# Optimization experiments

Measured on AMD Instinct MI355X. Metric: run time of the kernel, lower is better.

Reference implementation:

```python
import jax, jax.numpy as jnp
import numpy as np

N = 100000   # nodes
E = 1200000  # edges
D = 64       # emb_dim
XIN = 18     # x_dim + node_dim
XD = 16      # x_dim (output)
ED = 1       # edge_dim
L = 4        # num message-passing layers
G = 8        # graphs in batch (for global_mean_pool)


def setup_inputs() -> dict:
    key = jax.random.key(0)
    ks = iter(jax.random.split(key, 64))
    def nrm(shape, s=0.05):
        return jax.random.normal(next(ks), shape, dtype=jnp.float32) * s
    inp = {}
    inp["x"] = jax.random.normal(next(ks), (N, XIN), dtype=jnp.float32)
    inp["edge_attr"] = jax.random.normal(next(ks), (E, ED), dtype=jnp.float32)
    inp["W_in"] = nrm((XIN, D)); inp["b_in"] = jnp.zeros((D,), jnp.float32)
    # per-layer stacked params (leading dim L)
    inp["msg_W1"] = nrm((L, 2 * D + ED, D)); inp["msg_b1"] = jnp.zeros((L, D), jnp.float32)
    inp["msg_g1"] = jnp.ones((L, D), jnp.float32); inp["msg_be1"] = jnp.zeros((L, D), jnp.float32)
    inp["msg_W2"] = nrm((L, D, D)); inp["msg_b2"] = jnp.zeros((L, D), jnp.float32)
    inp["msg_g2"] = jnp.ones((L, D), jnp.float32); inp["msg_be2"] = jnp.zeros((L, D), jnp.float32)
    inp["upd_W1"] = nrm((L, 2 * D, D)); inp["upd_b1"] = jnp.zeros((L, D), jnp.float32)
    inp["upd_g1"] = jnp.ones((L, D), jnp.float32); inp["upd_be1"] = jnp.zeros((L, D), jnp.float32)
    inp["upd_W2"] = nrm((L, D, D)); inp["upd_b2"] = jnp.zeros((L, D), jnp.float32)
    inp["upd_g2"] = jnp.ones((L, D), jnp.float32); inp["upd_be2"] = jnp.zeros((L, D), jnp.float32)
    inp["reward_W"] = nrm((D, D)); inp["reward_b"] = jnp.zeros((D,), jnp.float32)
    inp["rout_W"] = nrm((D, 1)); inp["rout_b"] = jnp.zeros((1,), jnp.float32)
    inp["pred_W"] = nrm((D, D)); inp["pred_b"] = jnp.zeros((D,), jnp.float32)
    inp["pout_W"] = nrm((D, XD)); inp["pout_b"] = jnp.zeros((XD,), jnp.float32)
    inp["edge_index"] = jax.random.randint(next(ks), (2, E), 0, N)
    inp["batch"] = jnp.sort(jax.random.randint(next(ks), (N,), 0, G))
    return inp


def _bn(x, g, b, eps=1e-5):
    # BatchNorm1d in training mode: batch mean + biased variance
    m = jnp.mean(x, axis=0)
    v = jnp.mean((x - m) ** 2, axis=0)
    return (x - m) * jax.lax.rsqrt(v + eps) * g + b


def _mlp(x, W1, b1, g1, be1, W2, b2, g2, be2):
    h = jax.nn.relu(_bn(x @ W1 + b1, g1, be1))
    return jax.nn.relu(_bn(h @ W2 + b2, g2, be2))


def _forward(x, edge_attr, W_in, b_in,
             msg_W1, msg_b1, msg_g1, msg_be1, msg_W2, msg_b2, msg_g2, msg_be2,
             upd_W1, upd_b1, upd_g1, upd_be1, upd_W2, upd_b2, upd_g2, upd_be2,
             reward_W, reward_b, rout_W, rout_b, pred_W, pred_b, pout_W, pout_b,
             edge_index, batch):
    src = edge_index[0]  # j (source)
    dst = edge_index[1]  # i (target); PyG default flow source_to_target
    n = x.shape[0]
    h = x @ W_in + b_in
    for l in range(L):
        # message: gather + concat + MLP(psi)
        m = jnp.concatenate([h[dst], h[src], edge_attr], axis=-1)  # (E, 2D+ED)
        m = _mlp(m, msg_W1[l], msg_b1[l], msg_g1[l], msg_be1[l],
                 msg_W2[l], msg_b2[l], msg_g2[l], msg_be2[l])
        # aggregate: scatter-add to target nodes
        agg = jax.ops.segment_sum(m, dst, num_segments=n)  # (N, D)
        # update: concat + MLP(phi); residual add from outer network
        u = jnp.concatenate([h, agg], axis=-1)
        h = h + _mlp(u, upd_W1[l], upd_b1[l], upd_g1[l], upd_be1[l],
                     upd_W2[l], upd_b2[l], upd_g2[l], upd_be2[l])
    # reward head (computed in the original forward but not returned)
    h_reward = h @ reward_W + reward_b
    cnt = jax.ops.segment_sum(jnp.ones((n,), h.dtype), batch, num_segments=G)
    h_graph = jax.ops.segment_sum(h_reward, batch, num_segments=G) / jnp.maximum(cnt, 1.0)[:, None]
    _out_reward = h_graph @ rout_W + rout_b  # unused, matches original return
    # prediction head
    x_out = jax.nn.relu(h @ pred_W + pred_b) @ pout_W + pout_b  # (N, XD)
    return x_out


def reference(x, edge_attr, W_in, b_in,
              msg_W1, msg_b1, msg_g1, msg_be1, msg_W2, msg_b2, msg_g2, msg_be2,
              upd_W1, upd_b1, upd_g1, upd_be1, upd_W2, upd_b2, upd_g2, upd_be2,
              reward_W, reward_b, rout_W, rout_b, pred_W, pred_b, pout_W, pout_b,
              edge_index, batch):
    return _forward(x, edge_attr, W_in, b_in,
                    msg_W1, msg_b1, msg_g1, msg_be1, msg_W2, msg_b2, msg_g2, msg_be2,
                    upd_W1, upd_b1, upd_g1, upd_be1, upd_W2, upd_b2, upd_g2, upd_be2,
                    reward_W, reward_b, rout_W, rout_b, pred_W, pred_b, pout_W, pout_b,
                    edge_index, batch)
```

## Files before the change

kernel.cpp:

```cpp
#include <hip/hip_runtime.h>
#include <hip/hip_fp16.h>

typedef unsigned short u16;
typedef unsigned int u32;
typedef __attribute__((ext_vector_type(8))) unsigned short us8;
typedef __attribute__((ext_vector_type(8))) _Float16 f16x8;
typedef __attribute__((ext_vector_type(4))) float f32x4;

#define EPS 1e-5f

__device__ __forceinline__ float h2f(u16 h){ __half v; *(u16*)&v = h; return __half2float(v); }
__device__ __forceinline__ u16 f2h(float f){ __half v = __float2half(f); return *(u16*)&v; }

__global__ __launch_bounds__(256) void k_in(const float* __restrict__ x,
    const float* __restrict__ Win, const float* __restrict__ bin,
    float* __restrict__ h, int N){
  __shared__ float Ws[18][64];
  __shared__ float xs[64][20];
  int tid = threadIdx.x;
  for (int i = tid; i < 18*64; i += 256) Ws[i>>6][i&63] = Win[i];
  int row0 = blockIdx.x * 64;
  for (int i = tid; i < 64*18; i += 256){
    int r = i/18, k = i - r*18;
    int row = row0 + r;
    xs[r][k] = (row < N) ? x[(size_t)row*18 + k] : 0.f;
  }
  __syncthreads();
  int rq = tid >> 4, dq = tid & 15;
  float4 b4 = *(const float4*)(bin + dq*4);
  float acc[4][4];
  #pragma unroll
  for (int j=0;j<4;j++){ acc[j][0]=b4.x; acc[j][1]=b4.y; acc[j][2]=b4.z; acc[j][3]=b4.w; }
  for (int k=0;k<18;k++){
    float4 wv = *(const float4*)&Ws[k][dq*4];
    #pragma unroll
    for (int j=0;j<4;j++){
      float v = xs[rq*4+j][k];
      acc[j][0]+=v*wv.x; acc[j][1]+=v*wv.y; acc[j][2]+=v*wv.z; acc[j][3]+=v*wv.w;
    }
  }
  #pragma unroll
  for (int j=0;j<4;j++){
    int row = row0 + rq*4 + j;
    if (row < N)
      *(float4*)(h + (size_t)row*64 + dq*4) = make_float4(acc[j][0],acc[j][1],acc[j][2],acc[j][3]);
  }
}

__global__ __launch_bounds__(256) void k_pq(const float* __restrict__ h,
    const float* __restrict__ A, const float* __restrict__ B,
    u16* __restrict__ P, u16* __restrict__ Q, int N){
  __shared__ float hs[64][68];
  __shared__ float As[64][64];
  __shared__ float Bs[64][64];
  int tid = threadIdx.x;
  for (int i = tid; i < 4096; i += 256){ As[i>>6][i&63] = A[i]; Bs[i>>6][i&63] = B[i]; }
  int row0 = blockIdx.x*64;
  for (int i = tid; i < 4096; i += 256){
    int r = i>>6, k = i&63; int row = row0+r;
    hs[r][k] = (row<N)? h[(size_t)row*64+k] : 0.f;
  }
  __syncthreads();
  int rq = tid>>4, dq = tid&15;
  float ap[4][4]={}, aq[4][4]={};
  for (int k=0;k<64;k+=4){
    float4 hv[4];
    #pragma unroll
    for (int j=0;j<4;j++) hv[j] = *(const float4*)&hs[rq*4+j][k];
    #pragma unroll
    for (int kk=0;kk<4;kk++){
      float4 av = *(const float4*)&As[k+kk][dq*4];
      float4 bv = *(const float4*)&Bs[k+kk][dq*4];
      #pragma unroll
      for (int j=0;j<4;j++){
        float v = ((const float*)&hv[j])[kk];
        ap[j][0]+=v*av.x; ap[j][1]+=v*av.y; ap[j][2]+=v*av.z; ap[j][3]+=v*av.w;
        aq[j][0]+=v*bv.x; aq[j][1]+=v*bv.y; aq[j][2]+=v*bv.z; aq[j][3]+=v*bv.w;
      }
    }
  }
  #pragma unroll
  for (int j=0;j<4;j++){
    int row = row0 + rq*4 + j;
    if (row<N){
      ushort4 pk, qk;
      pk.x=f2h(ap[j][0]); pk.y=f2h(ap[j][1]); pk.z=f2h(ap[j][2]); pk.w=f2h(ap[j][3]);
      qk.x=f2h(aq[j][0]); qk.y=f2h(aq[j][1]); qk.z=f2h(aq[j][2]); qk.w=f2h(aq[j][3]);
      *(ushort4*)(P+(size_t)row*64+dq*4) = pk;
      *(ushort4*)(Q+(size_t)row*64+dq*4) = qk;
    }
  }
}

__global__ __launch_bounds__(256) void k_hist(const int* __restrict__ ei, int* __restrict__ cnt, int E){
  int e = blockIdx.x*256 + threadIdx.x;
  if (e < E) atomicAdd(&cnt[ei[E+e]], 1);
}

__global__ __launch_bounds__(256) void k_scan_a(const int* __restrict__ cnt, int* __restrict__ rp,
    int* __restrict__ bsum, int N){
  __shared__ int sm[256];
  int tid = threadIdx.x;
  int i0 = blockIdx.x*1024 + tid*4;
  int v0 = (i0+0<N)? cnt[i0+0]:0;
  int v1 = (i0+1<N)? cnt[i0+1]:0;
  int v2 = (i0+2<N)? cnt[i0+2]:0;
  int v3 = (i0+3<N)? cnt[i0+3]:0;
  int s = v0+v1+v2+v3;
  sm[tid] = s; __syncthreads();
  for (int ofs=1; ofs<256; ofs<<=1){
    int v = sm[tid];
    if (tid >= ofs) v += sm[tid-ofs];
    __syncthreads(); sm[tid] = v; __syncthreads();
  }
  int base = sm[tid] - s;
  int a0 = base+v0, a1 = a0+v1, a2 = a1+v2, a3 = a2+v3;
  if (i0+0<N) rp[i0+0]=a0;
  if (i0+1<N) rp[i0+1]=a1;
  if (i0+2<N) rp[i0+2]=a2;
  if (i0+3<N) rp[i0+3]=a3;
  if (tid==255) bsum[blockIdx.x] = sm[255];
}

__global__ void k_scan_b(int* __restrict__ bsum, int NB){
  if (threadIdx.x==0){
    int run = 0;
    for (int b=0;b<NB;b++){ int t = bsum[b]; bsum[b] = run; run += t; }
  }
}

__global__ __launch_bounds__(256) void k_scan_c(const int* __restrict__ cnt, int* __restrict__ rp,
    int* __restrict__ wr, const int* __restrict__ bsum, int N, int E){
  int tid = threadIdx.x;
  int i0 = blockIdx.x*1024 + tid*4;
  int off = bsum[blockIdx.x];
  #pragma unroll
  for (int j=0;j<4;j++){
    int i = i0+j;
    if (i<N){ int ex = off + rp[i] - cnt[i]; rp[i] = ex; wr[i] = ex; }
  }
  if (blockIdx.x==0 && tid==0) rp[N] = E;
}

__global__ __launch_bounds__(256) void k_perm(const int* __restrict__ ei, const float* __restrict__ ea,
    int* __restrict__ wr, int2* __restrict__ seS, int E){
  int e = blockIdx.x*256 + threadIdx.x;
  if (e < E){
    int dn = ei[E+e];
    int pos = atomicAdd(&wr[dn], 1);
    seS[pos] = make_int2(ei[e], __float_as_int(ea[e]));
  }
}

__global__ __launch_bounds__(256) void k_t1s(const u16* __restrict__ P, const u16* __restrict__ Q,
    const int2* __restrict__ seS, const int* __restrict__ rp,
    const float* __restrict__ c1, const float* __restrict__ b1,
    u16* __restrict__ t, float* __restrict__ stats, int N){
  int tid = threadIdx.x;
  int lane = tid & 63, w = tid >> 6;
  int sub = lane >> 5;
  int dl = (lane & 31) * 2;
  float cv0 = c1[dl], cv1 = c1[dl+1];
  float bv0 = b1[dl], bv1 = b1[dl+1];
  float s0 = 0.f, s1 = 0.f, qs0 = 0.f, qs1 = 0.f;
  for (int n = blockIdx.x*4 + w; n < N; n += gridDim.x*4){
    int a = rp[n], b = rp[n+1];
    u32 pp = *(const u32*)(P + (size_t)n*64 + dl);
    float p0 = h2f((u16)(pp & 0xffffu)) + bv0;
    float p1 = h2f((u16)(pp >> 16)) + bv1;
    int p = a + sub;
    for (; p + 2 < b; p += 4){
      int2 seA = seS[p];
      int2 seB = seS[p+2];
      u32 qA = *(const u32*)(Q + (size_t)seA.x*64 + dl);
      u32 qB = *(const u32*)(Q + (size_t)seB.x*64 + dl);
      float eaA = __int_as_float(seA.y), eaB = __int_as_float(seB.y);
      float tA0 = p0 + h2f((u16)(qA & 0xffffu)) + eaA*cv0;
      float tA1 = p1 + h2f((u16)(qA >> 16)) + eaA*cv1;
      float tB0 = p0 + h2f((u16)(qB & 0xffffu)) + eaB*cv0;
      float tB1 = p1 + h2f((u16)(qB >> 16)) + eaB*cv1;
      *(u32*)(t + (size_t)p*64 + dl) = (u32)f2h(tA0) | ((u32)f2h(tA1) << 16);
      *(u32*)(t + (size_t)(p+2)*64 + dl) = (u32)f2h(tB0) | ((u32)f2h(tB1) << 16);
      s0 += tA0 + tB0; s1 += tA1 + tB1;
      qs0 += tA0*tA0 + tB0*tB0; qs1 += tA1*tA1 + tB1*tB1;
    }
    for (; p < b; p += 2){
      int2 se = seS[p];
      u32 qq = *(const u32*)(Q + (size_t)se.x*64 + dl);
      float ea = __int_as_float(se.y);
      float t0 = p0 + h2f((u16)(qq & 0xffffu)) + ea*cv0;
      float t1 = p1 + h2f((u16)(qq >> 16)) + ea*cv1;
      *(u32*)(t + (size_t)p*64 + dl) = (u32)f2h(t0) | ((u32)f2h(t1) << 16);
      s0 += t0; s1 += t1; qs0 += t0*t0; qs1 += t1*t1;
    }
  }
  __shared__ float sS[8][64], qS[8][64];
  int idx = w*2 + sub;
  sS[idx][dl] = s0; sS[idx][dl+1] = s1;
  qS[idx][dl] = qs0; qS[idx][dl+1] = qs1;
  __syncthreads();
  if (tid < 64){
    float ts = 0.f, tq = 0.f;
    #pragma unroll
    for (int r=0;r<8;r++){ ts += sS[r][tid]; tq += qS[r][tid]; }
    atomicAdd(&stats[tid], ts);
    atomicAdd(&stats[64+tid], tq);
  }
}

__global__ __launch_bounds__(256) void k_m2s(u16* __restrict__ t,
    const float* __restrict__ g1, const float* __restrict__ be1, const float* __restrict__ stats1,
    const float* __restrict__ W2, const float* __restrict__ b2,
    float* __restrict__ stats2, int E, float invE){
  __shared__ _Float16 yL[128][72];
  __shared__ _Float16 wL[64][72];
  __shared__ float scS[64], shS[64], b2S[64];
  int tid = threadIdx.x;
  if (tid < 64){
    float m = stats1[tid]*invE;
    float v = stats1[64+tid]*invE - m*m;
    float sc = g1[tid]*rsqrtf(v + EPS);
    scS[tid] = sc; shS[tid] = be1[tid] - m*sc;
    b2S[tid] = b2[tid];
  }
  for (int i = tid; i < 4096; i += 256){
    int k = i >> 6, n = i & 63;
    wL[n][k] = (_Float16)W2[i];
  }
  __syncthreads();
  int lane = tid & 63, wv = tid >> 6;
  int arow = lane & 15;
  int kgrp = lane >> 4;
  int srow = tid >> 1, sc0 = (tid & 1)*32;
  float ssum[4] = {}, ssq[4] = {};
  int ntiles = (E + 127) >> 7;
  for (int tile = blockIdx.x; tile < ntiles; tile += gridDim.x){
    int e0 = tile << 7;
    {
      int p = e0 + srow;
      if (p < E){
        const u16* src = t + (size_t)p*64 + sc0;
        #pragma unroll
        for (int c=0;c<4;c++){
          f16x8 a = *(const f16x8*)(src + c*8);
          f16x8 v;
          #pragma unroll
          for (int j=0;j<8;j++){
            int dd = sc0 + c*8 + j;
            v[j] = (_Float16)fmaxf((float)a[j]*scS[dd] + shS[dd], 0.f);
          }
          *(f16x8*)&yL[srow][sc0 + c*8] = v;
        }
      } else {
        f16x8 z;
        #pragma unroll
        for (int j=0;j<8;j++) z[j] = (_Float16)0.f;
        #pragma unroll
        for (int c=0;c<4;c++) *(f16x8*)&yL[srow][sc0 + c*8] = z;
      }
    }
    __syncthreads();
    f32x4 acc[2][4];
    #pragma unroll
    for (int mf=0; mf<2; mf++){
      int row = 32*wv + 16*mf + arow;
      f16x8 a0 = *(const f16x8*)&yL[row][8*kgrp];
      f16x8 a1 = *(const f16x8*)&yL[row][32 + 8*kgrp];
      #pragma unroll
      for (int c=0;c<4;c++){
        f16x8 b0 = *(const f16x8*)&wL[16*c + arow][8*kgrp];
        f16x8 b1 = *(const f16x8*)&wL[16*c + arow][32 + 8*kgrp];
        f32x4 d = {0.f,0.f,0.f,0.f};
        d = __builtin_amdgcn_mfma_f32_16x16x32_f16(a0, b0, d, 0, 0, 0);
        d = __builtin_amdgcn_mfma_f32_16x16x32_f16(a1, b1, d, 0, 0, 0);
        acc[mf][c] = d;
      }
    }
    __syncthreads();
    #pragma unroll
    for (int mf=0; mf<2; mf++){
      #pragma unroll
      for (int c=0;c<4;c++){
        int col = 16*c + arow;
        float bb = b2S[col];
        #pragma unroll
        for (int r=0;r<4;r++){
          int e = e0 + 32*wv + 16*mf + 4*kgrp + r;
          if (e < E){
            float v = acc[mf][c][r] + bb;
            t[(size_t)e*64 + col] = f2h(v);
            ssum[c] += v; ssq[c] += v*v;
          }
        }
      }
    }
  }
  __syncthreads();
  float* red = (float*)yL;
  #pragma unroll
  for (int c=0;c<4;c++) red[c*256 + tid] = ssum[c];
  __syncthreads();
  if (tid < 64){
    int cc = tid >> 4;
    float s = 0.f;
    for (int g=0; g<16; g++) s += red[cc*256 + g*16 + (tid & 15)];
    atomicAdd(&stats2[tid], s);
  }
  __syncthreads();
  #pragma unroll
  for (int c=0;c<4;c++) red[c*256 + tid] = ssq[c];
  __syncthreads();
  if (tid < 64){
    int cc = tid >> 4;
    float s = 0.f;
    for (int g=0; g<16; g++) s += red[cc*256 + g*16 + (tid & 15)];
    atomicAdd(&stats2[64+tid], s);
  }
}

__global__ __launch_bounds__(256) void k_agg(const u16* __restrict__ t2, const int* __restrict__ rp,
    const float* __restrict__ g2, const float* __restrict__ be2, const float* __restrict__ stats2,
    float* __restrict__ agg, int N, float invE){
  __shared__ float scS[64], shS[64];
  int tid = threadIdx.x;
  if (tid < 64){
    float m = stats2[tid]*invE;
    float v = stats2[64+tid]*invE - m*m;
    float sc = g2[tid]*rsqrtf(v+EPS);
    scS[tid] = sc; shS[tid] = be2[tid] - m*sc;
  }
  __syncthreads();
  int lane = tid & 63, w = tid >> 6;
  int sub = lane >> 5;
  int dl = (lane & 31) * 2;
  float sc0 = scS[dl], sc1 = scS[dl+1], sh0 = shS[dl], sh1 = shS[dl+1];
  for (int n = blockIdx.x*4 + w; n < N; n += gridDim.x*4){
    int a = rp[n], b = rp[n+1];
    float a0 = 0.f, a1 = 0.f;
    int p = a + sub;
    for (; p + 2 < b; p += 4){
      u32 vA = *(const u32*)(t2 + (size_t)p*64 + dl);
      u32 vB = *(const u32*)(t2 + (size_t)(p+2)*64 + dl);
      a0 += fmaxf(h2f((u16)(vA & 0xffffu))*sc0 + sh0, 0.f)
          + fmaxf(h2f((u16)(vB & 0xffffu))*sc0 + sh0, 0.f);
      a1 += fmaxf(h2f((u16)(vA >> 16))*sc1 + sh1, 0.f)
          + fmaxf(h2f((u16)(vB >> 16))*sc1 + sh1, 0.f);
    }
    for (; p < b; p += 2){
      u32 vA = *(const u32*)(t2 + (size_t)p*64 + dl);
      a0 += fmaxf(h2f((u16)(vA & 0xffffu))*sc0 + sh0, 0.f);
      a1 += fmaxf(h2f((u16)(vA >> 16))*sc1 + sh1, 0.f);
    }
    a0 += __shfl_xor(a0, 32);
    a1 += __shfl_xor(a1, 32);
    if (sub == 0)
      *(float2*)(agg + (size_t)n*64 + dl) = make_float2(a0, a1);
  }
}

__global__ __launch_bounds__(256) void k_s1(const u16* __restrict__ P, const u16* __restrict__ Q,
    const float* __restrict__ ea, const int* __restrict__ ei,
    const float* __restrict__ c1, const float* __restrict__ b1,
    float* __restrict__ stats, int E){
  int tid = threadIdx.x;
  int d = tid & 63, w = tid >> 6;
  float cv = c1[d], bv = b1[d];
  float s = 0.f, sq = 0.f;
  for (int e = blockIdx.x*4 + w; e < E; e += gridDim.x*4){
    int dn = ei[E+e], sn = ei[e];
    float t = h2f(P[(size_t)dn*64+d]) + h2f(Q[(size_t)sn*64+d]) + ea[e]*cv + bv;
    s += t; sq += t*t;
  }
  __shared__ float sS[4][64], qS[4][64];
  sS[w][d] = s; qS[w][d] = sq;
  __syncthreads();
  if (tid < 64){
    float ts = sS[0][tid]+sS[1][tid]+sS[2][tid]+sS[3][tid];
    float tq = qS[0][tid]+qS[1][tid]+qS[2][tid]+qS[3][tid];
    atomicAdd(&stats[tid], ts);
    atomicAdd(&stats[64+tid], tq);
  }
}

__global__ __launch_bounds__(256) void k_m2b(const u16* __restrict__ P, const u16* __restrict__ Q,
    const float* __restrict__ ea, const int* __restrict__ ei,
    const float* __restrict__ c1, const float* __restrict__ b1,
    const float* __restrict__ g1, const float* __restrict__ be1,
    const float* __restrict__ stats1,
    const float* __restrict__ W2, const float* __restrict__ b2,
    float* __restrict__ stats2, int E, float invE){
  __shared__ float ys[64][68];
  __shared__ float Ws[64][64];
  __shared__ float scS[64], c1S[64], bS[64], b2S[64];
  int tid = threadIdx.x;
  if (tid < 64){
    float m = stats1[tid]*invE;
    float v = stats1[64+tid]*invE - m*m;
    float sc = g1[tid]*rsqrtf(v + EPS);
    float sh = be1[tid] - m*sc;
    scS[tid] = sc;
    c1S[tid] = c1[tid]*sc;
    bS[tid]  = b1[tid]*sc + sh;
    b2S[tid] = b2[tid];
  }
  for (int i=tid;i<4096;i+=256) Ws[i>>6][i&63] = W2[i];
  __syncthreads();
  int rq = tid>>4, dq = tid&15;
  float ssum[4]={}, ssq[4]={};
  int ntiles = (E+63)>>6;
  for (int tile = blockIdx.x; tile < ntiles; tile += gridDim.x){
    int e0 = tile<<6;
    for (int i = tid; i < 4096; i += 256){
      int el = i>>6, dd = i&63;
      int e = e0 + el;
      float y = 0.f;
      if (e < E){
        int dn = ei[E+e], sn = ei[e];
        float t = (h2f(P[(size_t)dn*64+dd]) + h2f(Q[(size_t)sn*64+dd]))*scS[dd] + ea[e]*c1S[dd] + bS[dd];
        y = fmaxf(t, 0.f);
      }
      ys[el][dd] = y;
    }
    __syncthreads();
    float acc[4][4];
    float4 b4 = *(const float4*)&b2S[dq*4];
    #pragma unroll
    for (int j=0;j<4;j++){ acc[j][0]=b4.x; acc[j][1]=b4.y; acc[j][2]=b4.z; acc[j][3]=b4.w; }
    for (int k=0;k<64;k+=4){
      float4 hv[4];
      #pragma unroll
      for (int j=0;j<4;j++) hv[j] = *(const float4*)&ys[rq*4+j][k];
      #pragma unroll
      for (int kk=0;kk<4;kk++){
        float4 wv = *(const float4*)&Ws[k+kk][dq*4];
        #pragma unroll
        for (int j=0;j<4;j++){
          float v = ((const float*)&hv[j])[kk];
          acc[j][0]+=v*wv.x; acc[j][1]+=v*wv.y; acc[j][2]+=v*wv.z; acc[j][3]+=v*wv.w;
        }
      }
    }
    #pragma unroll
    for (int j=0;j<4;j++){
      int e = e0 + rq*4 + j;
      if (e < E){
        #pragma unroll
        for (int c=0;c<4;c++){ float v=acc[j][c]; ssum[c]+=v; ssq[c]+=v*v; }
      }
    }
    __syncthreads();
  }
  float* red = &ys[0][0];
  #pragma unroll
  for (int c=0;c<4;c++) red[rq*64 + dq*4 + c] = ssum[c];
  __syncthreads();
  if (tid < 64){
    float t=0.f;
    for (int r=0;r<16;r++) t += red[r*64+tid];
    atomicAdd(&stats2[tid], t);
  }
  __syncthreads();
  #pragma unroll
  for (int c=0;c<4;c++) red[rq*64 + dq*4 + c] = ssq[c];
  __syncthreads();
  if (tid < 64){
    float t=0.f;
    for (int r=0;r<16;r++) t += red[r*64+tid];
    atomicAdd(&stats2[64+tid], t);
  }
}

__global__ __launch_bounds__(256) void k_sc_rec(const u16* __restrict__ P, const u16* __restrict__ Q,
    const float* __restrict__ ea, const int* __restrict__ ei,
    const float* __restrict__ c1, const float* __restrict__ b1,
    const float* __restrict__ g1, const float* __restrict__ be1, const float* __restrict__ stats1,
    const float* __restrict__ W2, const float* __restrict__ b2,
    const float* __restrict__ g2, const float* __restrict__ be2, const float* __restrict__ stats2,
    float* __restrict__ agg, int E, float invE){
  __shared__ float ys[64][68];
  __shared__ float Ws[64][64];
  __shared__ float scS[64], c1S[64], bS[64];
  __shared__ float s2S[64], h2S[64], b2S[64];
  int tid = threadIdx.x;
  if (tid < 64){
    float m = stats1[tid]*invE;
    float v = stats1[64+tid]*invE - m*m;
    float sc = g1[tid]*rsqrtf(v + EPS);
    scS[tid] = sc;
    c1S[tid] = c1[tid]*sc;
    bS[tid]  = b1[tid]*sc + be1[tid] - m*sc;
    float m2 = stats2[tid]*invE;
    float v2 = stats2[64+tid]*invE - m2*m2;
    float sc2 = g2[tid]*rsqrtf(v2+EPS);
    s2S[tid] = sc2; h2S[tid] = be2[tid] - m2*sc2;
    b2S[tid] = b2[tid];
  }
  for (int i=tid;i<4096;i+=256) Ws[i>>6][i&63] = W2[i];
  __syncthreads();
  int rq = tid>>4, dq = tid&15;
  int ntiles = (E+63)>>6;
  for (int tile = blockIdx.x; tile < ntiles; tile += gridDim.x){
    int e0 = tile<<6;
    for (int i = tid; i < 4096; i += 256){
      int el = i>>6, dd = i&63;
      int e = e0 + el;
      float y = 0.f;
      if (e < E){
        int dn = ei[E+e], sn = ei[e];
        float t = (h2f(P[(size_t)dn*64+dd]) + h2f(Q[(size_t)sn*64+dd]))*scS[dd] + ea[e]*c1S[dd] + bS[dd];
        y = fmaxf(t, 0.f);
      }
      ys[el][dd] = y;
    }
    __syncthreads();
    float acc[4][4];
    float4 b4 = *(const float4*)&b2S[dq*4];
    #pragma unroll
    for (int j=0;j<4;j++){ acc[j][0]=b4.x; acc[j][1]=b4.y; acc[j][2]=b4.z; acc[j][3]=b4.w; }
    for (int k=0;k<64;k+=4){
      float4 hv[4];
      #pragma unroll
      for (int j=0;j<4;j++) hv[j] = *(const float4*)&ys[rq*4+j][k];
      #pragma unroll
      for (int kk=0;kk<4;kk++){
        float4 wv = *(const float4*)&Ws[k+kk][dq*4];
        #pragma unroll
        for (int j=0;j<4;j++){
          float v = ((const float*)&hv[j])[kk];
          acc[j][0]+=v*wv.x; acc[j][1]+=v*wv.y; acc[j][2]+=v*wv.z; acc[j][3]+=v*wv.w;
        }
      }
    }
    float4 sc4 = *(const float4*)&s2S[dq*4];
    float4 sh4 = *(const float4*)&h2S[dq*4];
    #pragma unroll
    for (int j=0;j<4;j++){
      int e = e0 + rq*4 + j;
      if (e < E){
        int dn = ei[E+e];
        float y0 = fmaxf(acc[j][0]*sc4.x + sh4.x, 0.f);
        float y1 = fmaxf(acc[j][1]*sc4.y + sh4.y, 0.f);
        float y2 = fmaxf(acc[j][2]*sc4.z + sh4.z, 0.f);
        float y3 = fmaxf(acc[j][3]*sc4.w + sh4.w, 0.f);
        atomicAdd(&agg[(size_t)dn*64 + dq*4    ], y0);
        atomicAdd(&agg[(size_t)dn*64 + dq*4 + 1], y1);
        atomicAdd(&agg[(size_t)dn*64 + dq*4 + 2], y2);
        atomicAdd(&agg[(size_t)dn*64 + dq*4 + 3], y3);
      }
    }
    __syncthreads();
  }
}

__global__ __launch_bounds__(256) void k_up1(const float* __restrict__ h, const float* __restrict__ agg,
    const float* __restrict__ U1, const float* __restrict__ b1u,
    float* __restrict__ tn, float* __restrict__ stats3, int N){
  __shared__ float ins[64][68];
  __shared__ float Ws[64][64];
  int tid = threadIdx.x;
  int rq = tid>>4, dq = tid&15;
  int row0 = blockIdx.x*64;
  float4 b4 = *(const float4*)(b1u + dq*4);
  float acc[4][4];
  #pragma unroll
  for (int j=0;j<4;j++){ acc[j][0]=b4.x; acc[j][1]=b4.y; acc[j][2]=b4.z; acc[j][3]=b4.w; }
  for (int p=0;p<2;p++){
    const float* src = p ? agg : h;
    for (int i=tid;i<4096;i+=256){
      int r=i>>6,k=i&63; int row=row0+r;
      ins[r][k] = (row<N)? src[(size_t)row*64+k] : 0.f;
    }
    for (int i=tid;i<4096;i+=256) Ws[i>>6][i&63] = U1[p*4096 + i];
    __syncthreads();
    for (int k=0;k<64;k+=4){
      float4 hv[4];
      #pragma unroll
      for (int j=0;j<4;j++) hv[j] = *(const float4*)&ins[rq*4+j][k];
      #pragma unroll
      for (int kk=0;kk<4;kk++){
        float4 wv = *(const float4*)&Ws[k+kk][dq*4];
        #pragma unroll
        for (int j=0;j<4;j++){
          float v = ((const float*)&hv[j])[kk];
          acc[j][0]+=v*wv.x; acc[j][1]+=v*wv.y; acc[j][2]+=v*wv.z; acc[j][3]+=v*wv.w;
        }
      }
    }
    __syncthreads();
  }
  float ssum[4]={}, ssq[4]={};
  #pragma unroll
  for (int j=0;j<4;j++){
    int row = row0 + rq*4 + j;
    if (row<N){
      *(float4*)(tn+(size_t)row*64+dq*4) = make_float4(acc[j][0],acc[j][1],acc[j][2],acc[j][3]);
      #pragma unroll
      for (int c=0;c<4;c++){ float v=acc[j][c]; ssum[c]+=v; ssq[c]+=v*v; }
    }
  }
  float* red = &ins[0][0];
  #pragma unroll
  for (int c=0;c<4;c++) red[rq*64 + dq*4 + c] = ssum[c];
  __syncthreads();
  if (tid < 64){
    float t=0.f; for (int r=0;r<16;r++) t += red[r*64+tid];
    atomicAdd(&stats3[tid], t);
  }
  __syncthreads();
  #pragma unroll
  for (int c=0;c<4;c++) red[rq*64 + dq*4 + c] = ssq[c];
  __syncthreads();
  if (tid < 64){
    float t=0.f; for (int r=0;r<16;r++) t += red[r*64+tid];
    atomicAdd(&stats3[64+tid], t);
  }
}

__global__ __launch_bounds__(256) void k_up2(float* __restrict__ tn,
    const float* __restrict__ g3, const float* __restrict__ be3, const float* __restrict__ stats3,
    const float* __restrict__ U2, const float* __restrict__ b2u,
    float* __restrict__ stats4, int N, float invN){
  __shared__ float ys[64][68];
  __shared__ float Ws[64][64];
  __shared__ float scS[64], shS[64], bS[64];
  int tid = threadIdx.x;
  if (tid < 64){
    float m = stats3[tid]*invN;
    float v = stats3[64+tid]*invN - m*m;
    float sc = g3[tid]*rsqrtf(v+EPS);
    scS[tid] = sc; shS[tid] = be3[tid] - m*sc; bS[tid] = b2u[tid];
  }
  for (int i=tid;i<4096;i+=256) Ws[i>>6][i&63] = U2[i];
  int row0 = blockIdx.x*64;
  __syncthreads();
  for (int i=tid;i<4096;i+=256){
    int r=i>>6,k=i&63; int row=row0+r;
    float y = 0.f;
    if (row<N) y = fmaxf(tn[(size_t)row*64+k]*scS[k] + shS[k], 0.f);
    ys[r][k] = y;
  }
  __syncthreads();
  int rq = tid>>4, dq = tid&15;
  float4 b4 = *(const float4*)&bS[dq*4];
  float acc[4][4];
  #pragma unroll
  for (int j=0;j<4;j++){ acc[j][0]=b4.x; acc[j][1]=b4.y; acc[j][2]=b4.z; acc[j][3]=b4.w; }
  for (int k=0;k<64;k+=4){
    float4 hv[4];
    #pragma unroll
    for (int j=0;j<4;j++) hv[j] = *(const float4*)&ys[rq*4+j][k];
    #pragma unroll
    for (int kk=0;kk<4;kk++){
      float4 wv = *(const float4*)&Ws[k+kk][dq*4];
      #pragma unroll
      for (int j=0;j<4;j++){
        float v = ((const float*)&hv[j])[kk];
        acc[j][0]+=v*wv.x; acc[j][1]+=v*wv.y; acc[j][2]+=v*wv.z; acc[j][3]+=v*wv.w;
      }
    }
  }
  float ssum[4]={}, ssq[4]={};
  #pragma unroll
  for (int j=0;j<4;j++){
    int row = row0 + rq*4 + j;
    if (row<N){
      *(float4*)(tn+(size_t)row*64+dq*4) = make_float4(acc[j][0],acc[j][1],acc[j][2],acc[j][3]);
      #pragma unroll
      for (int c=0;c<4;c++){ float v=acc[j][c]; ssum[c]+=v; ssq[c]+=v*v; }
    }
  }
  __syncthreads();
  float* red = &ys[0][0];
  #pragma unroll
  for (int c=0;c<4;c++) red[rq*64 + dq*4 + c] = ssum[c];
  __syncthreads();
  if (tid < 64){
    float t=0.f; for (int r=0;r<16;r++) t += red[r*64+tid];
    atomicAdd(&stats4[tid], t);
  }
  __syncthreads();
  #pragma unroll
  for (int c=0;c<4;c++) red[rq*64 + dq*4 + c] = ssq[c];
  __syncthreads();
  if (tid < 64){
    float t=0.f; for (int r=0;r<16;r++) t += red[r*64+tid];
    atomicAdd(&stats4[64+tid], t);
  }
}

__global__ __launch_bounds__(256) void k_res_pq(float* __restrict__ h, const float* __restrict__ tn,
    const float* __restrict__ g4, const float* __restrict__ be4, const float* __restrict__ stats4,
    const float* __restrict__ A, const float* __restrict__ B,
    u16* __restrict__ P, u16* __restrict__ Q, int N, float invN){
  __shared__ float hs[64][68];
  __shared__ float As[64][64];
  __shared__ float Bs[64][64];
  __shared__ float scS[64], shS[64];
  int tid = threadIdx.x;
  if (tid < 64){
    float m = stats4[tid]*invN;
    float v = stats4[64+tid]*invN - m*m;
    float sc = g4[tid]*rsqrtf(v+EPS);
    scS[tid] = sc; shS[tid] = be4[tid] - m*sc;
  }
  for (int i = tid; i < 4096; i += 256){ As[i>>6][i&63] = A[i]; Bs[i>>6][i&63] = B[i]; }
  int row0 = blockIdx.x*64;
  __syncthreads();
  for (int i = tid; i < 4096; i += 256){
    int r = i>>6, k = i&63; int row = row0+r;
    float hv = 0.f;
    if (row<N){
      hv = h[(size_t)row*64+k] + fmaxf(tn[(size_t)row*64+k]*scS[k] + shS[k], 0.f);
      h[(size_t)row*64+k] = hv;
    }
    hs[r][k] = hv;
  }
  __syncthreads();
  int rq = tid>>4, dq = tid&15;
  float ap[4][4]={}, aq[4][4]={};
  for (int k=0;k<64;k+=4){
    float4 hv[4];
    #pragma unroll
    for (int j=0;j<4;j++) hv[j] = *(const float4*)&hs[rq*4+j][k];
    #pragma unroll
    for (int kk=0;kk<4;kk++){
      float4 av = *(const float4*)&As[k+kk][dq*4];
      float4 bv = *(const float4*)&Bs[k+kk][dq*4];
      #pragma unroll
      for (int j=0;j<4;j++){
        float v = ((const float*)&hv[j])[kk];
        ap[j][0]+=v*av.x; ap[j][1]+=v*av.y; ap[j][2]+=v*av.z; ap[j][3]+=v*av.w;
        aq[j][0]+=v*bv.x; aq[j][1]+=v*bv.y; aq[j][2]+=v*bv.z; aq[j][3]+=v*bv.w;
      }
    }
  }
  #pragma unroll
  for (int j=0;j<4;j++){
    int row = row0 + rq*4 + j;
    if (row<N){
      ushort4 pk, qk;
      pk.x=f2h(ap[j][0]); pk.y=f2h(ap[j][1]); pk.z=f2h(ap[j][2]); pk.w=f2h(ap[j][3]);
      qk.x=f2h(aq[j][0]); qk.y=f2h(aq[j][1]); qk.z=f2h(aq[j][2]); qk.w=f2h(aq[j][3]);
      *(ushort4*)(P+(size_t)row*64+dq*4) = pk;
      *(ushort4*)(Q+(size_t)row*64+dq*4) = qk;
    }
  }
}

__global__ __launch_bounds__(256) void k_res_head(const float* __restrict__ h, const float* __restrict__ tn,
    const float* __restrict__ g4, const float* __restrict__ be4, const float* __restrict__ stats4,
    const float* __restrict__ Wp, const float* __restrict__ bp,
    const float* __restrict__ Wo, const float* __restrict__ bo,
    float* __restrict__ out, int N, float invN){
  __shared__ float hs[64][68];
  __shared__ float Wps[64][64];
  __shared__ float ps[64][68];
  __shared__ float Wos[64][16];
  __shared__ float scS[64], shS[64];
  int tid = threadIdx.x;
  if (tid < 64){
    float m = stats4[tid]*invN;
    float v = stats4[64+tid]*invN - m*m;
    float sc = g4[tid]*rsqrtf(v+EPS);
    scS[tid] = sc; shS[tid] = be4[tid] - m*sc;
  }
  for (int i=tid;i<4096;i+=256) Wps[i>>6][i&63] = Wp[i];
  for (int i=tid;i<1024;i+=256) Wos[i>>4][i&15] = Wo[i];
  int row0 = blockIdx.x*64;
  __syncthreads();
  for (int i = tid; i < 4096; i += 256){
    int r = i>>6, k = i&63; int row = row0+r;
    float hv = 0.f;
    if (row<N)
      hv = h[(size_t)row*64+k] + fmaxf(tn[(size_t)row*64+k]*scS[k] + shS[k], 0.f);
    hs[r][k] = hv;
  }
  __syncthreads();
  int rq = tid>>4, dq = tid&15;
  float4 b4 = *(const float4*)(bp + dq*4);
  float acc[4][4];
  #pragma unroll
  for (int j=0;j<4;j++){ acc[j][0]=b4.x; acc[j][1]=b4.y; acc[j][2]=b4.z; acc[j][3]=b4.w; }
  for (int k=0;k<64;k+=4){
    float4 hv[4];
    #pragma unroll
    for (int j=0;j<4;j++) hv[j] = *(const float4*)&hs[rq*4+j][k];
    #pragma unroll
    for (int kk=0;kk<4;kk++){
      float4 wv = *(const float4*)&Wps[k+kk][dq*4];
      #pragma unroll
      for (int j=0;j<4;j++){
        float v = ((const float*)&hv[j])[kk];
        acc[j][0]+=v*wv.x; acc[j][1]+=v*wv.y; acc[j][2]+=v*wv.z; acc[j][3]+=v*wv.w;
      }
    }
  }
  #pragma unroll
  for (int j=0;j<4;j++){
    *(float4*)&ps[rq*4+j][dq*4] = make_float4(fmaxf(acc[j][0],0.f), fmaxf(acc[j][1],0.f),
                                              fmaxf(acc[j][2],0.f), fmaxf(acc[j][3],0.f));
  }
  __syncthreads();
  int f = tid & 15;
  float bof = bo[f];
  float acc2[4] = {bof, bof, bof, bof};
  for (int k=0;k<64;k++){
    float wv = Wos[k][f];
    #pragma unroll
    for (int j=0;j<4;j++) acc2[j] += ps[rq*4+j][k]*wv;
  }
  #pragma unroll
  for (int j=0;j<4;j++){
    int row = row0 + rq*4 + j;
    if (row<N) out[(size_t)row*16 + f] = acc2[j];
  }
}

extern "C" void kernel_launch(void* const* d_in, const int* in_sizes, int n_in,
                              void* d_out, int out_size, void* d_ws, size_t ws_size,
                              hipStream_t stream){
  const float* x    = (const float*)d_in[0];
  const float* eatt = (const float*)d_in[1];
  const float* Win  = (const float*)d_in[2];
  const float* bin  = (const float*)d_in[3];
  const float* mW1  = (const float*)d_in[4];
  const float* mb1  = (const float*)d_in[5];
  const float* mg1  = (const float*)d_in[6];
  const float* mbe1 = (const float*)d_in[7];
  const float* mW2  = (const float*)d_in[8];
  const float* mb2  = (const float*)d_in[9];
  const float* mg2  = (const float*)d_in[10];
  const float* mbe2 = (const float*)d_in[11];
  const float* uW1  = (const float*)d_in[12];
  const float* ub1  = (const float*)d_in[13];
  const float* ug1  = (const float*)d_in[14];
  const float* ube1 = (const float*)d_in[15];
  const float* uW2  = (const float*)d_in[16];
  const float* ub2  = (const float*)d_in[17];
  const float* ug2  = (const float*)d_in[18];
  const float* ube2 = (const float*)d_in[19];
  const float* predW = (const float*)d_in[24];
  const float* predb = (const float*)d_in[25];
  const float* poutW = (const float*)d_in[26];
  const float* poutb = (const float*)d_in[27];
  const int*   ei    = (const int*)d_in[28];

  const int N = in_sizes[0] / 18;
  const int E = in_sizes[1];

  size_t nodeB = (size_t)N * 64 * sizeof(float);
  size_t halfB = (size_t)N * 64 * sizeof(u16);
  size_t t2B   = (size_t)E * 64 * sizeof(u16);
  size_t statsB = 16 * 128 * sizeof(float);
  int NB = (N + 1023)/1024;
  size_t csrB = (size_t)E*8 + (size_t)(N+1)*4 + (size_t)N*4 + (size_t)N*4 + 4096*4;

  bool planA = ws_size >= nodeB + 2*halfB + nodeB + t2B + csrB + statsB;

  char* w = (char*)d_ws;
  float* h = (float*)w; w += nodeB;
  u16* P = (u16*)w; w += halfB;
  u16* Q = (u16*)w; w += halfB;
  float* agg = (float*)w; w += nodeB;
  float* tn = agg;
  u16*  t2 = nullptr;
  int2* seS = nullptr;
  int *rp=nullptr, *cnt=nullptr, *wrp=nullptr, *bsum=nullptr;
  float* stats;
  if (planA){
    t2   = (u16*)w;  w += t2B;
    seS  = (int2*)w; w += (size_t)E*8;
    rp   = (int*)w;  w += (size_t)(N+1)*4;
    cnt  = (int*)w;  w += (size_t)N*4;
    wrp  = (int*)w;  w += (size_t)N*4;
    bsum = (int*)w;  w += 4096*4;
    stats = (float*)w;
  } else {
    stats = (float*)w;
  }

  hipMemsetAsync(stats, 0, statsB, stream);

  int nb = (N + 63)/64;
  float invE = 1.0f/(float)E, invN = 1.0f/(float)N;

  k_in<<<nb, 256, 0, stream>>>(x, Win, bin, h, N);
  k_pq<<<nb, 256, 0, stream>>>(h, mW1, mW1 + 4096, P, Q, N);

  if (planA){
    hipMemsetAsync(cnt, 0, (size_t)N*4, stream);
    k_hist<<<(E+255)/256, 256, 0, stream>>>(ei, cnt, E);
    k_scan_a<<<NB, 256, 0, stream>>>(cnt, rp, bsum, N);
    k_scan_b<<<1, 64, 0, stream>>>(bsum, NB);
    k_scan_c<<<NB, 256, 0, stream>>>(cnt, rp, wrp, bsum, N, E);
    k_perm<<<(E+255)/256, 256, 0, stream>>>(ei, eatt, wrp, seS, E);
  }

  for (int l = 0; l < 4; ++l){
    float* s1 = stats + (l*4+0)*128;
    float* s2 = stats + (l*4+1)*128;
    float* s3 = stats + (l*4+2)*128;
    float* s4 = stats + (l*4+3)*128;
    const float* A  = mW1 + (size_t)l*8256;
    const float* c1 = A + 8192;
    if (planA){
      k_t1s<<<2048, 256, 0, stream>>>(P, Q, seS, rp, c1, mb1 + l*64, t2, s1, N);
      k_m2s<<<2048, 256, 0, stream>>>(t2, mg1 + l*64, mbe1 + l*64, s1,
                                      mW2 + (size_t)l*4096, mb2 + l*64, s2, E, invE);
      k_agg<<<2048, 256, 0, stream>>>(t2, rp, mg2 + l*64, mbe2 + l*64, s2, agg, N, invE);
    } else {
      k_s1<<<2048, 256, 0, stream>>>(P, Q, eatt, ei, c1, mb1 + l*64, s1, E);
      k_m2b<<<1024, 256, 0, stream>>>(P, Q, eatt, ei, c1, mb1 + l*64, mg1 + l*64, mbe1 + l*64,
                                      s1, mW2 + (size_t)l*4096, mb2 + l*64, s2, E, invE);
      hipMemsetAsync(agg, 0, nodeB, stream);
      k_sc_rec<<<1024, 256, 0, stream>>>(P, Q, eatt, ei, c1, mb1 + l*64, mg1 + l*64, mbe1 + l*64,
                                         s1, mW2 + (size_t)l*4096, mb2 + l*64,
                                         mg2 + l*64, mbe2 + l*64, s2, agg, E, invE);
    }
    k_up1<<<nb, 256, 0, stream>>>(h, agg, uW1 + (size_t)l*8192, ub1 + l*64, tn, s3, N);
    k_up2<<<nb, 256, 0, stream>>>(tn, ug1 + l*64, ube1 + l*64, s3, uW2 + (size_t)l*4096,
                                  ub2 + l*64, s4, N, invN);
    if (l < 3){
      const float* An = mW1 + (size_t)(l+1)*8256;
      k_res_pq<<<nb, 256, 0, stream>>>(h, tn, ug2 + l*64, ube2 + l*64, s4,
                                       An, An + 4096, P, Q, N, invN);
    } else {
      k_res_head<<<nb, 256, 0, stream>>>(h, tn, ug2 + l*64, ube2 + l*64, s4,
                                         predW, predb, poutW, poutb, (float*)d_out, N, invN);
    }
  }
}
```

Before: 2.166 ms.

## Port node update and P/Q projection kernels to fp16 MFMA

Rewrites k_up1, k_up2 and k_res_pq to stage inputs and transposed weights in LDS as fp16 and compute the 64x64 GEMMs with 16x16x32 MFMA instructions instead of scalar fp32 FMAs. Loads are vectorized per row, and the BN stats reduction is remapped to the MFMA output layout. This cuts ALU time in the node-side kernels. In exchange it adds fp16 rounding of h/agg inputs and weights, and it leaves the dominant edge-message kernel unchanged.

```diff
diff --git a/kernel.cpp b/kernel.cpp
--- a/kernel.cpp
+++ b/kernel.cpp
@@ -11,6 +11,7 @@
 
 __device__ __forceinline__ float h2f(u16 h){ __half v; *(u16*)&v = h; return __half2float(v); }
 __device__ __forceinline__ u16 f2h(float f){ __half v = __float2half(f); return *(u16*)&v; }
+__device__ __forceinline__ u32 pkh(float a, float b){ return (u32)f2h(a) | ((u32)f2h(b) << 16); }
 
 __global__ __launch_bounds__(256) void k_in(const float* __restrict__ x,
     const float* __restrict__ Win, const float* __restrict__ bin,
@@ -555,64 +556,87 @@
 __global__ __launch_bounds__(256) void k_up1(const float* __restrict__ h, const float* __restrict__ agg,
     const float* __restrict__ U1, const float* __restrict__ b1u,
     float* __restrict__ tn, float* __restrict__ stats3, int N){
-  __shared__ float ins[64][68];
-  __shared__ float Ws[64][64];
-  int tid = threadIdx.x;
-  int rq = tid>>4, dq = tid&15;
-  int row0 = blockIdx.x*64;
-  float4 b4 = *(const float4*)(b1u + dq*4);
-  float acc[4][4];
-  #pragma unroll
-  for (int j=0;j<4;j++){ acc[j][0]=b4.x; acc[j][1]=b4.y; acc[j][2]=b4.z; acc[j][3]=b4.w; }
-  for (int p=0;p<2;p++){
-    const float* src = p ? agg : h;
-    for (int i=tid;i<4096;i+=256){
-      int r=i>>6,k=i&63; int row=row0+r;
-      ins[r][k] = (row<N)? src[(size_t)row*64+k] : 0.f;
-    }
-    for (int i=tid;i<4096;i+=256) Ws[i>>6][i&63] = U1[p*4096 + i];
-    __syncthreads();
-    for (int k=0;k<64;k+=4){
-      float4 hv[4];
-      #pragma unroll
-      for (int j=0;j<4;j++) hv[j] = *(const float4*)&ins[rq*4+j][k];
-      #pragma unroll
-      for (int kk=0;kk<4;kk++){
-        float4 wv = *(const float4*)&Ws[k+kk][dq*4];
-        #pragma unroll
-        for (int j=0;j<4;j++){
-          float v = ((const float*)&hv[j])[kk];
-          acc[j][0]+=v*wv.x; acc[j][1]+=v*wv.y; acc[j][2]+=v*wv.z; acc[j][3]+=v*wv.w;
-        }
-      }
-    }
-    __syncthreads();
-  }
+  __shared__ _Float16 yL[64][136];
+  __shared__ _Float16 wL[64][136];
+  __shared__ float bS[64];
+  int tid = threadIdx.x;
+  if (tid < 64) bS[tid] = b1u[tid];
+  for (int i = tid; i < 8192; i += 256){
+    int k = i >> 6, n = i & 63;
+    wL[n][k] = (_Float16)U1[i];
+  }
+  int row0 = blockIdx.x * 64;
+  int srow = tid >> 2, sc0 = (tid & 3) * 16;
+  {
+    int row = row0 + srow;
+    if (row < N){
+      #pragma unroll
+      for (int c=0;c<4;c++){
+        float4 v = *(const float4*)(h + (size_t)row*64 + sc0 + 4*c);
+        *(u32*)&yL[srow][sc0+4*c]   = pkh(v.x, v.y);
+        *(u32*)&yL[srow][sc0+4*c+2] = pkh(v.z, v.w);
+      }
+      #pragma unroll
+      for (int c=0;c<4;c++){
+        float4 v = *(const float4*)(agg + (size_t)row*64 + sc0 + 4*c);
+        *(u32*)&yL[srow][64+sc0+4*c]   = pkh(v.x, v.y);
+        *(u32*)&yL[srow][64+sc0+4*c+2] = pkh(v.z, v.w);
+      }
+    } else {
+      #pragma unroll
+      for (int c=0;c<4;c++){
+        *(u32*)&yL[srow][sc0+4*c] = 0u; *(u32*)&yL[srow][sc0+4*c+2] = 0u;
+        *(u32*)&yL[srow][64+sc0+4*c] = 0u; *(u32*)&yL[srow][64+sc0+4*c+2] = 0u;
+      }
+    }
+  }
+  __syncthreads();
+  int lane = tid & 63, wv = tid >> 6;
+  int arow = lane & 15, kgrp = lane >> 4;
+  f16x8 a[4];
+  #pragma unroll
+  for (int kk=0;kk<4;kk++) a[kk] = *(const f16x8*)&yL[16*wv + arow][32*kk + 8*kgrp];
   float ssum[4]={}, ssq[4]={};
   #pragma unroll
-  for (int j=0;j<4;j++){
-    int row = row0 + rq*4 + j;
-    if (row<N){
-      *(float4*)(tn+(size_t)row*64+dq*4) = make_float4(acc[j][0],acc[j][1],acc[j][2],acc[j][3]);
-      #pragma unroll
-      for (int c=0;c<4;c++){ float v=acc[j][c]; ssum[c]+=v; ssq[c]+=v*v; }
-    }
-  }
-  float* red = &ins[0][0];
-  #pragma unroll
-  for (int c=0;c<4;c++) red[rq*64 + dq*4 + c] = ssum[c];
-  __syncthreads();
-  if (tid < 64){
-    float t=0.f; for (int r=0;r<16;r++) t += red[r*64+tid];
-    atomicAdd(&stats3[tid], t);
-  }
-  __syncthreads();
-  #pragma unroll
-  for (int c=0;c<4;c++) red[rq*64 + dq*4 + c] = ssq[c];
-  __syncthreads();
-  if (tid < 64){
-    float t=0.f; for (int r=0;r<16;r++) t += red[r*64+tid];
-    atomicAdd(&stats3[64+tid], t);
+  for (int c=0;c<4;c++){
+    f32x4 d = {0.f,0.f,0.f,0.f};
+    #pragma unroll
+    for (int kk=0;kk<4;kk++){
+      f16x8 b = *(const f16x8*)&wL[16*c + arow][32*kk + 8*kgrp];
+      d = __builtin_amdgcn_mfma_f32_16x16x32_f16(a[kk], b, d, 0, 0, 0);
+    }
+    int col = 16*c + arow;
+    float bb = bS[col];
+    #pragma unroll
+    for (int r=0;r<4;r++){
+      int row = row0 + 16*wv + 4*kgrp + r;
+      if (row < N){
+        float v = d[r] + bb;
+        tn[(size_t)row*64 + col] = v;
+        ssum[c]+=v; ssq[c]+=v*v;
+      }
+    }
+  }
+  __syncthreads();
+  float* red = (float*)yL;
+  #pragma unroll
+  for (int c=0;c<4;c++) red[c*256 + tid] = ssum[c];
+  __syncthreads();
+  if (tid < 64){
+    int cc = tid >> 4;
+    float s = 0.f;
+    for (int g=0; g<16; g++) s += red[cc*256 + g*16 + (tid & 15)];
+    atomicAdd(&stats3[tid], s);
+  }
+  __syncthreads();
+  #pragma unroll
+  for (int c=0;c<4;c++) red[c*256 + tid] = ssq[c];
+  __syncthreads();
+  if (tid < 64){
+    int cc = tid >> 4;
+    float s = 0.f;
+    for (int g=0; g<16; g++) s += red[cc*256 + g*16 + (tid & 15)];
+    atomicAdd(&stats3[64+tid], s);
   }
 }
 
@@ -620,8 +644,8 @@
     const float* __restrict__ g3, const float* __restrict__ be3, const float* __restrict__ stats3,
     const float* __restrict__ U2, const float* __restrict__ b2u,
     float* __restrict__ stats4, int N, float invN){
-  __shared__ float ys[64][68];
-  __shared__ float Ws[64][64];
+  __shared__ _Float16 yL[64][72];
+  __shared__ _Float16 wL[64][72];
   __shared__ float scS[64], shS[64], bS[64];
   int tid = threadIdx.x;
   if (tid < 64){
@@ -630,61 +654,79 @@
     float sc = g3[tid]*rsqrtf(v+EPS);
     scS[tid] = sc; shS[tid] = be3[tid] - m*sc; bS[tid] = b2u[tid];
   }
-  for (int i=tid;i<4096;i+=256) Ws[i>>6][i&63] = U2[i];
-  int row0 = blockIdx.x*64;
-  __syncthreads();
-  for (int i=tid;i<4096;i+=256){
-    int r=i>>6,k=i&63; int row=row0+r;
-    float y = 0.f;
-    if (row<N) y = fmaxf(tn[(size_t)row*64+k]*scS[k] + shS[k], 0.f);
-    ys[r][k] = y;
-  }
-  __syncthreads();
-  int rq = tid>>4, dq = tid&15;
-  float4 b4 = *(const float4*)&bS[dq*4];
-  float acc[4][4];
-  #pragma unroll
-  for (int j=0;j<4;j++){ acc[j][0]=b4.x; acc[j][1]=b4.y; acc[j][2]=b4.z; acc[j][3]=b4.w; }
-  for (int k=0;k<64;k+=4){
-    float4 hv[4];
-    #pragma unroll
-    for (int j=0;j<4;j++) hv[j] = *(const float4*)&ys[rq*4+j][k];
-    #pragma unroll
-    for (int kk=0;kk<4;kk++){
-      float4 wv = *(const float4*)&Ws[k+kk][dq*4];
-      #pragma unroll
-      for (int j=0;j<4;j++){
-        float v = ((const float*)&hv[j])[kk];
-        acc[j][0]+=v*wv.x; acc[j][1]+=v*wv.y; acc[j][2]+=v*wv.z; acc[j][3]+=v*wv.w;
-      }
-    }
-  }
+  for (int i = tid; i < 4096; i += 256){
+    int k = i >> 6, n = i & 63;
+    wL[n][k] = (_Float16)U2[i];
+  }
+  __syncthreads();
+  int row0 = blockIdx.x * 64;
+  int srow = tid >> 2, sc0 = (tid & 3) * 16;
+  {
+    int row = row0 + srow;
+    if (row < N){
+      #pragma unroll
+      for (int c=0;c<4;c++){
+        float4 v = *(const float4*)(tn + (size_t)row*64 + sc0 + 4*c);
+        int d0 = sc0 + 4*c;
+        float y0 = fmaxf(v.x*scS[d0  ] + shS[d0  ], 0.f);
+        float y1 = fmaxf(v.y*scS[d0+1] + shS[d0+1], 0.f);
+        float y2 = fmaxf(v.z*scS[d0+2] + shS[d0+2], 0.f);
+        float y3 = fmaxf(v.w*scS[d0+3] + shS[d0+3], 0.f);
+        *(u32*)&yL[srow][d0]   = pkh(y0, y1);
+        *(u32*)&yL[srow][d0+2] = pkh(y2, y3);
+      }
+    } else {
+      #pragma unroll
+      for (int c=0;c<4;c++){
+        *(u32*)&yL[srow][sc0+4*c] = 0u; *(u32*)&yL[srow][sc0+4*c+2] = 0u;
+      }
+    }
+  }
+  __syncthreads();
+  int lane = tid & 63, wv = tid >> 6;
+  int arow = lane & 15, kgrp = lane >> 4;
+  f16x8 a0 = *(const f16x8*)&yL[16*wv + arow][8*kgrp];
+  f16x8 a1 = *(const f16x8*)&yL[16*wv + arow][32 + 8*kgrp];
   float ssum[4]={}, ssq[4]={};
   #pragma unroll
-  for (int j=0;j<4;j++){
-    int row = row0 + rq*4 + j;
-    if (row<N){
-      *(float4*)(tn+(size_t)row*64+dq*4) = make_float4(acc[j][0],acc[j][1],acc[j][2],acc[j][3]);
-      #pragma unroll
-      for (int c=0;c<4;c++){ float v=acc[j][c]; ssum[c]+=v; ssq[c]+=v*v; }
-    }
-  }
-  __syncthreads();
-  float* red = &ys[0][0];
-  #pragma unroll
-  for (int c=0;c<4;c++) red[rq*64 + dq*4 + c] = ssum[c];
-  __syncthreads();
-  if (tid < 64){
-    float t=0.f; for (int r=0;r<16;r++) t += red[r*64+tid];
-    atomicAdd(&stats4[tid], t);
-  }
-  __syncthreads();
-  #pragma unroll
-  for (int c=0;c<4;c++) red[rq*64 + dq*4 + c] = ssq[c];
-  __syncthreads();
-  if (tid < 64){
-    float t=0.f; for (int r=0;r<16;r++) t += red[r*64+tid];
-    atomicAdd(&stats4[64+tid], t);
+  for (int c=0;c<4;c++){
+    f16x8 b0 = *(const f16x8*)&wL[16*c + arow][8*kgrp];
+    f16x8 b1 = *(const f16x8*)&wL[16*c + arow][32 + 8*kgrp];
+    f32x4 d = {0.f,0.f,0.f,0.f};
+    d = __builtin_amdgcn_mfma_f32_16x16x32_f16(a0, b0, d, 0, 0, 0);
+    d = __builtin_amdgcn_mfma_f32_16x16x32_f16(a1, b1, d, 0, 0, 0);
+    int col = 16*c + arow;
+    float bb = bS[col];
+    #pragma unroll
+    for (int r=0;r<4;r++){
+      int row = row0 + 16*wv + 4*kgrp + r;
+      if (row < N){
+        float v = d[r] + bb;
+        tn[(size_t)row*64 + col] = v;
+        ssum[c]+=v; ssq[c]+=v*v;
+      }
+    }
+  }
+  __syncthreads();
+  float* red = (float*)yL;
+  #pragma unroll
+  for (int c=0;c<4;c++) red[c*256 + tid] = ssum[c];
+  __syncthreads();
+  if (tid < 64){
+    int cc = tid >> 4;
+    float s = 0.f;
+    for (int g=0; g<16; g++) s += red[cc*256 + g*16 + (tid & 15)];
+    atomicAdd(&stats4[tid], s);
+  }
+  __syncthreads();
+  #pragma unroll
+  for (int c=0;c<4;c++) red[c*256 + tid] = ssq[c];
+  __syncthreads();
+  if (tid < 64){
+    int cc = tid >> 4;
+    float s = 0.f;
+    for (int g=0; g<16; g++) s += red[cc*256 + g*16 + (tid & 15)];
+    atomicAdd(&stats4[64+tid], s);
   }
 }
 
@@ -692,9 +734,9 @@
     const float* __restrict__ g4, const float* __restrict__ be4, const float* __restrict__ stats4,
     const float* __restrict__ A, const float* __restrict__ B,
     u16* __restrict__ P, u16* __restrict__ Q, int N, float invN){
-  __shared__ float hs[64][68];
-  __shared__ float As[64][64];
-  __shared__ float Bs[64][64];
+  __shared__ _Float16 yL[64][72];
+  __shared__ _Float16 wLa[64][72];
+  __shared__ _Float16 wLb[64][72];
   __shared__ float scS[64], shS[64];
   int tid = threadIdx.x;
   if (tid < 64){
@@ -703,46 +745,61 @@
     float sc = g4[tid]*rsqrtf(v+EPS);
     scS[tid] = sc; shS[tid] = be4[tid] - m*sc;
   }
-  for (int i = tid; i < 4096; i += 256){ As[i>>6][i&63] = A[i]; Bs[i>>6][i&63] = B[i]; }
-  int row0 = blockIdx.x*64;
-  __syncthreads();
   for (int i = tid; i < 4096; i += 256){
-    int r = i>>6, k = i&63; int row = row0+r;
-    float hv = 0.f;
-    if (row<N){
-      hv = h[(size_t)row*64+k] + fmaxf(tn[(size_t)row*64+k]*scS[k] + shS[k], 0.f);
-      h[(size_t)row*64+k] = hv;
-    }
-    hs[r][k] = hv;
-  }
-  __syncthreads();
-  int rq = tid>>4, dq = tid&15;
-  float ap[4][4]={}, aq[4][4]={};
-  for (int k=0;k<64;k+=4){
-    float4 hv[4];
-    #pragma unroll
-    for (int j=0;j<4;j++) hv[j] = *(const float4*)&hs[rq*4+j][k];
-    #pragma unroll
-    for (int kk=0;kk<4;kk++){
-      float4 av = *(const float4*)&As[k+kk][dq*4];
-      float4 bv = *(const float4*)&Bs[k+kk][dq*4];
-      #pragma unroll
-      for (int j=0;j<4;j++){
-        float v = ((const float*)&hv[j])[kk];
-        ap[j][0]+=v*av.x; ap[j][1]+=v*av.y; ap[j][2]+=v*av.z; ap[j][3]+=v*av.w;
-        aq[j][0]+=v*bv.x; aq[j][1]+=v*bv.y; aq[j][2]+=v*bv.z; aq[j][3]+=v*bv.w;
-      }
-    }
-  }
-  #pragma unroll
-  for (int j=0;j<4;j++){
-    int row = row0 + rq*4 + j;
-    if (row<N){
-      ushort4 pk, qk;
-      pk.x=f2h(ap[j][0]); pk.y=f2h(ap[j][1]); pk.z=f2h(ap[j][2]); pk.w=f2h(ap[j][3]);
-      qk.x=f2h(aq[j][0]); qk.y=f2h(aq[j][1]); qk.z=f2h(aq[j][2]); qk.w=f2h(aq[j][3]);
-      *(ushort4*)(P+(size_t)row*64+dq*4) = pk;
-      *(ushort4*)(Q+(size_t)row*64+dq*4) = qk;
+    int k = i >> 6, n = i & 63;
+    wLa[n][k] = (_Float16)A[i];
+    wLb[n][k] = (_Float16)B[i];
+  }
+  __syncthreads();
+  int row0 = blockIdx.x * 64;
+  int srow = tid >> 2, sc0 = (tid & 3) * 16;
+  {
+    int row = row0 + srow;
+    if (row < N){
+      #pragma unroll
+      for (int c=0;c<4;c++){
+        int d0 = sc0 + 4*c;
+        float4 hv4 = *(const float4*)(h + (size_t)row*64 + d0);
+        float4 tv4 = *(const float4*)(tn + (size_t)row*64 + d0);
+        float h0 = hv4.x + fmaxf(tv4.x*scS[d0  ] + shS[d0  ], 0.f);
+        float h1 = hv4.y + fmaxf(tv4.y*scS[d0+1] + shS[d0+1], 0.f);
+        float h2 = hv4.z + fmaxf(tv4.z*scS[d0+2] + shS[d0+2], 0.f);
+        float h3 = hv4.w + fmaxf(tv4.w*scS[d0+3] + shS[d0+3], 0.f);
+        *(float4*)(h + (size_t)row*64 + d0) = make_float4(h0,h1,h2,h3);
+        *(u32*)&yL[srow][d0]   = pkh(h0, h1);
+        *(u32*)&yL[srow][d0+2] = pkh(h2, h3);
+      }
+    } else {
+      #pragma unroll
+      for (int c=0;c<4;c++){
+        *(u32*)&yL[srow][sc0+4*c] = 0u; *(u32*)&yL[srow][sc0+4*c+2] = 0u;
+      }
+    }
+  }
+  __syncthreads();
+  int lane = tid & 63, wv = tid >> 6;
+  int arow = lane & 15, kgrp = lane >> 4;
+  f16x8 y0 = *(const f16x8*)&yL[16*wv + arow][8*kgrp];
+  f16x8 y1 = *(const f16x8*)&yL[16*wv + arow][32 + 8*kgrp];
+  int node = row0 + 16*wv + arow;
+  #pragma unroll
+  for (int c=0;c<4;c++){
+    f16x8 wa0 = *(const f16x8*)&wLa[16*c + arow][8*kgrp];
+    f16x8 wa1 = *(const f16x8*)&wLa[16*c + arow][32 + 8*kgrp];
+    f32x4 dp = {0.f,0.f,0.f,0.f};
+    dp = __builtin_amdgcn_mfma_f32_16x16x32_f16(wa0, y0, dp, 0, 0, 0);
+    dp = __builtin_amdgcn_mfma_f32_16x16x32_f16(wa1, y1, dp, 0, 0, 0);
+    f16x8 wb0 = *(const f16x8*)&wLb[16*c + arow][8*kgrp];
+    f16x8 wb1 = *(const f16x8*)&wLb[16*c + arow][32 + 8*kgrp];
+    f32x4 dq = {0.f,0.f,0.f,0.f};
+    dq = __builtin_amdgcn_mfma_f32_16x16x32_f16(wb0, y0, dq, 0, 0, 0);
+    dq = __builtin_amdgcn_mfma_f32_16x16x32_f16(wb1, y1, dq, 0, 0, 0);
+    if (node < N){
+      ushort4 pk4, qk4;
+      pk4.x = f2h(dp[0]); pk4.y = f2h(dp[1]); pk4.z = f2h(dp[2]); pk4.w = f2h(dp[3]);
+      qk4.x = f2h(dq[0]); qk4.y = f2h(dq[1]); qk4.z = f2h(dq[2]); qk4.w = f2h(dq[3]);
+      *(ushort4*)(P + (size_t)node*64 + 16*c + 4*kgrp) = pk4;
+      *(ushort4*)(Q + (size_t)node*64 + 16*c + 4*kgrp) = qk4;
     }
   }
 }
```

Result: faster. 1.929 ms (-11.0%).
